# Optimization experiments

Measured on AMD Instinct MI355X. Metric: run time of the kernel, lower is better.

Reference implementation:

```python
import jax, jax.numpy as jnp
import numpy as np

B = 2048       # batch
N = 256        # num_memory_locations
M = 64         # memory_size
U = 512        # num_units
IN = 10        # num_bits_per_vector + 2
SHIFT = 1      # conv_shift_range
CLIP = 20.0


def setup_inputs() -> dict:
    key = jax.random.key(0)
    ks = jax.random.split(key, 20)
    s = 0.05
    A0 = jax.random.uniform(ks[5], (2, B, N), dtype=jnp.float32)
    A0 = A0 / jnp.sum(A0, axis=-1, keepdims=True)  # distribution-like prev attention
    return {
        'x_t':  jax.random.normal(ks[0], (B, IN), dtype=jnp.float32),
        'H0':   jax.random.normal(ks[1], (B, U), dtype=jnp.float32) * s,
        'C0':   jax.random.normal(ks[2], (B, U), dtype=jnp.float32) * s,
        'm0':   jax.random.normal(ks[3], (B, N, M), dtype=jnp.float32) * s,
        'R0':   jax.random.normal(ks[4], (B, M), dtype=jnp.float32) * s,
        'A0':   A0,
        'Wprep': jax.random.normal(ks[6], (M, U), dtype=jnp.float32) * s,
        'bprep': jnp.zeros((U,), dtype=jnp.float32),
        'Wx':   jax.random.normal(ks[7], (IN + U, 4 * U), dtype=jnp.float32) * s,
        'Wh':   jax.random.normal(ks[8], (U, 4 * U), dtype=jnp.float32) * s,
        'bl':   jnp.zeros((4 * U,), dtype=jnp.float32),
        'Wr':   jax.random.normal(ks[9], (U, M + 6), dtype=jnp.float32) * s,
        'br':   jnp.zeros((M + 6,), dtype=jnp.float32),
        'Ww':   jax.random.normal(ks[10], (U, 3 * M + 6), dtype=jnp.float32) * s,
        'bw':   jnp.zeros((3 * M + 6,), dtype=jnp.float32),
        'Wo':   jax.random.normal(ks[11], (U + M, U), dtype=jnp.float32) * s,
        'bo':   jnp.zeros((U,), dtype=jnp.float32),
    }


def _addressing(head, m_tm1, a_tm1):
    # head: (B, >=M+6); m_tm1: (B,N,M); a_tm1: (B,N)
    k = jnp.tanh(head[:, :M])                                   # (B,M)
    beta = jax.nn.softplus(head[:, M])                          # (B,)
    g = jax.nn.sigmoid(head[:, M + 1])                          # (B,)
    s = jax.nn.softmax(head[:, M + 2:M + 2 + 2 * SHIFT + 1], axis=-1)  # (B,3)
    gamma = jax.nn.softplus(head[:, M + 2 + 2 * SHIFT + 1])     # (B,)
    # cosine similarity content addressing
    ip = jnp.einsum('bnm,bm->bn', m_tm1, k)                     # (B,N)
    k_norm = jnp.sqrt(jnp.sum(k * k, axis=1, keepdims=True))    # (B,1)
    m_norm = jnp.sqrt(jnp.sum(m_tm1 * m_tm1, axis=2))           # (B,N)
    K = ip / (k_norm * m_norm + 1e-8)
    w_c = jax.nn.softmax(beta[:, None] * K, axis=1)             # exp/sum == softmax
    w_g = g[:, None] * w_c + (1.0 - g[:, None]) * a_tm1
    # circular convolution: s placed at offsets [0..SHIFT] and [-SHIFT..-1]
    s_full = jnp.concatenate(
        [s[:, :SHIFT + 1], jnp.zeros((s.shape[0], N - (2 * SHIFT + 1)), s.dtype), s[:, -SHIFT:]],
        axis=1)                                                 # (B,N)
    idx = (jnp.arange(N)[:, None] - jnp.arange(N)[None, :]) % N  # (N,N)
    w_conv = jnp.einsum('bij,bj->bi', s_full[:, idx], w_g)       # w[i]=sum_j w_g[j]*s[(i-j)%N]
    w_sharp = w_conv ** gamma[:, None]
    return w_sharp / jnp.sum(w_sharp, axis=1, keepdims=True)


def reference(x_t, H0, C0, m0, R0, A0, Wprep, bprep, Wx, Wh, bl, Wr, br, Ww, bw, Wo, bo):
    # prep from previous reads
    h = R0 @ Wprep + bprep                                      # (B,U)
    # single-layer LSTM controller
    z = jnp.concatenate([x_t, h], axis=1) @ Wx + H0 @ Wh + bl   # (B,4U)
    i, f, g_, o = jnp.split(z, 4, axis=1)
    c_t = jax.nn.sigmoid(f) * C0 + jax.nn.sigmoid(i) * jnp.tanh(g_)
    h = jax.nn.sigmoid(o) * jnp.tanh(c_t)
    h = jnp.clip(h, -CLIP, CLIP)
    # heads
    r_out = h @ Wr + br                                         # (B, M+6)
    w_out = h @ Ww + bw                                         # (B, 3M+6)
    w_read = _addressing(r_out, m0, A0[0])                      # (B,N)
    w_write = _addressing(w_out, m0, A0[1])                     # (B,N)
    # read from OLD memory (as in original)
    R_t = jnp.einsum('bn,bnm->bm', w_read, m0)                  # (B,M)
    # write: erase + add
    del_v = jax.nn.sigmoid(w_out[:, -2 * M:-M])                 # (B,M)
    add_v = jnp.tanh(w_out[:, -M:])                             # (B,M)
    ww = w_write[:, :, None]                                    # (B,N,1)
    m_t = m0 * (1.0 - ww * del_v[:, None, :]) + ww * add_v[:, None, :]
    y_t = jnp.clip(jnp.concatenate([h, R_t], axis=1) @ Wo + bo, -CLIP, CLIP)
    return (y_t, m_t, R_t, w_read, w_write)
```

## Files before the change

kernel.cpp:

```cpp
#include <hip/hip_runtime.h>


using u16   = unsigned short;
using bfrag = __attribute__((ext_vector_type(8))) short;
using f4    = __attribute__((ext_vector_type(4))) float;

__device__ __forceinline__ float bf2f(u16 s){ union{float f;unsigned u;}v; v.u=((unsigned)s)<<16; return v.f; }
__device__ __forceinline__ u16 f2bf(float f){ union{float f;unsigned u;}v; v.f=f; unsigned r=v.u+0x7fffu+((v.u>>16)&1u); return (u16)(r>>16); }
__device__ __forceinline__ void bfpair(unsigned pr, float&a, float&b){ union{float f;unsigned u;}x,y; x.u=pr<<16; y.u=pr&0xffff0000u; a=x.f; b=y.f; }
__device__ __forceinline__ unsigned packbf(float a, float b){ return (unsigned)f2bf(a) | ((unsigned)f2bf(b)<<16); }
__device__ __forceinline__ float sigm(float x){ return 1.f/(1.f+expf(-x)); }
__device__ __forceinline__ float softplus_(float x){ return fmaxf(x,0.f)+log1pf(expf(-fabsf(x))); }

__device__ __forceinline__ void gld16(const u16* g, u16* l){
    __builtin_amdgcn_global_load_lds((const __attribute__((address_space(1))) unsigned*)g,
                                     (__attribute__((address_space(3))) unsigned*)l, 16, 0, 0);
}


__global__ __launch_bounds__(256) void k_wt_lstm(const float* __restrict__ Wx, const float* __restrict__ Wh,
                                                 u16* __restrict__ Wt){
    __shared__ float t[32][33];
    int n0 = blockIdx.x*32, k0 = blockIdx.y*32;
    int tx = threadIdx.x & 31, ty = threadIdx.x >> 5;
    #pragma unroll
    for(int r=0;r<4;r++){
        int k = k0 + ty*4 + r, n = n0 + tx;
        float v;
        if(k < 522)       v = Wx[k*2048 + n];
        else if(k < 1034) v = Wh[(k-522)*2048 + n];
        else              v = 0.f;
        t[ty*4+r][tx] = v;
    }
    __syncthreads();
    #pragma unroll
    for(int r=0;r<4;r++){
        int n = n0 + ty*4 + r, k = k0 + tx;
        Wt[n*1056 + k] = f2bf(t[tx][ty*4+r]);
    }
}

__global__ __launch_bounds__(256) void k_wt_heads(const float* __restrict__ Wr, const float* __restrict__ Ww,
                                                  u16* __restrict__ Wt){
    __shared__ float t[32][33];
    int n0 = blockIdx.x*32, k0 = blockIdx.y*32;
    int tx = threadIdx.x & 31, ty = threadIdx.x >> 5;
    #pragma unroll
    for(int r=0;r<4;r++){
        int k = k0 + ty*4 + r, n = n0 + tx;
        float v;
        if(n < 70)        v = Wr[k*70 + n];
        else if(n < 268)  v = Ww[k*198 + (n-70)];
        else              v = 0.f;
        t[ty*4+r][tx] = v;
    }
    __syncthreads();
    #pragma unroll
    for(int r=0;r<4;r++){
        int n = n0 + ty*4 + r, k = k0 + tx;
        Wt[n*512 + k] = f2bf(t[tx][ty*4+r]);
    }
}

__global__ __launch_bounds__(256) void k_wt_out(const float* __restrict__ Wo, u16* __restrict__ Wt){
    __shared__ float t[32][33];
    int n0 = blockIdx.x*32, k0 = blockIdx.y*32;
    int tx = threadIdx.x & 31, ty = threadIdx.x >> 5;
    #pragma unroll
    for(int r=0;r<4;r++){
        int k = k0 + ty*4 + r, n = n0 + tx;
        t[ty*4+r][tx] = Wo[k*512 + n];
    }
    __syncthreads();
    #pragma unroll
    for(int r=0;r<4;r++){
        int n = n0 + ty*4 + r, k = k0 + tx;
        Wt[n*576 + k] = f2bf(t[tx][ty*4+r]);
    }
}

__global__ __launch_bounds__(256) void k_abuild(const float* __restrict__ x, const float* __restrict__ H0,
                                                const float* __restrict__ R0, const float* __restrict__ Wprep,
                                                const float* __restrict__ bprep, u16* __restrict__ A){
    int flat = blockIdx.x*256 + threadIdx.x;
    int b = flat >> 9, u = flat & 511;
    u16* Ab = A + (size_t)b*1056;
    float acc = bprep[u];
    const float* r = R0 + b*64;
    #pragma unroll 8
    for(int m=0;m<64;m++) acc += r[m] * Wprep[m*512+u];
    Ab[10+u] = f2bf(acc);
    Ab[522+u] = f2bf(H0[b*512+u]);
    if(u<10) Ab[u] = f2bf(x[b*10+u]);
    if(u<22) Ab[1034+u] = 0;
}

__device__ __forceinline__ void gemm128(const u16* __restrict__ A, int lda,
                                        const u16* __restrict__ Bt, int ldb,
                                        int bm, int bn, int kiters,
                                        u16* Al, u16* Bl, f4 acc[4][4]){
    int tid = threadIdx.x, w = tid>>6, lane = tid&63, quad = lane>>4, l16 = lane&15;
    int wr = w>>1, wc = w&1;
    f4 z4 = {0.f,0.f,0.f,0.f};
    #pragma unroll
    for(int i=0;i<4;i++)
        #pragma unroll
        for(int j=0;j<4;j++) acc[i][j] = z4;
    int rA0 = tid>>2, kc = tid&3;
    int rA1 = rA0 + 64;
    const u16* ga0 = A  + (size_t)(bm+rA0)*lda + kc*8;
    const u16* ga1 = A  + (size_t)(bm+rA1)*lda + kc*8;
    const u16* gb0 = Bt + (size_t)(bn+rA0)*ldb + kc*8;
    const u16* gb1 = Bt + (size_t)(bn+rA1)*ldb + kc*8;
    u16* lA0 = Al + (w*64)*8;
    u16* lA1 = Al + (256 + w*64)*8;
    u16* lB0 = Bl + (w*64)*8;
    u16* lB1 = Bl + (256 + w*64)*8;
    for(int kt=0; kt<kiters; kt++){
        __syncthreads();
        gld16(ga0, lA0); gld16(ga1, lA1);
        gld16(gb0, lB0); gld16(gb1, lB1);
        ga0 += 32; ga1 += 32; gb0 += 32; gb1 += 32;
        __syncthreads();
        bfrag af[4], bf[4];
        #pragma unroll
        for(int i=0;i<4;i++) af[i] = *(const bfrag*)&Al[(wr*64 + i*16 + l16)*32 + quad*8];
        #pragma unroll
        for(int j=0;j<4;j++) bf[j] = *(const bfrag*)&Bl[(wc*64 + j*16 + l16)*32 + quad*8];
        #pragma unroll
        for(int i=0;i<4;i++)
            #pragma unroll
            for(int j=0;j<4;j++)
                acc[i][j] = __builtin_amdgcn_mfma_f32_16x16x32_bf16(af[i], bf[j], acc[i][j], 0, 0, 0);
    }
}

__global__ __launch_bounds__(256) void k_gemm_lstm(const u16* __restrict__ A, const u16* __restrict__ Wt,
                                                   float* __restrict__ z){
    __shared__ u16 Al[128*32], Bl[128*32];
    f4 acc[4][4];
    int bm = blockIdx.x*128, bn = blockIdx.y*128;
    gemm128(A, 1056, Wt, 1056, bm, bn, 33, Al, Bl, acc);
    int lane = threadIdx.x&63, quad = lane>>4, l16 = lane&15, w = threadIdx.x>>6;
    int wr = w>>1, wc = w&1;
    #pragma unroll
    for(int i=0;i<4;i++){
        #pragma unroll
        for(int j=0;j<4;j++){
            int col = bn + wc*64 + j*16 + l16;
            #pragma unroll
            for(int r=0;r<4;r++){
                int row = bm + wr*64 + i*16 + quad*4 + r;
                z[(size_t)row*2048 + col] = acc[i][j][r];
            }
        }
    }
}

__global__ __launch_bounds__(256) void k_gates(const float* __restrict__ z, const float* __restrict__ C0,
                                               const float* __restrict__ bl, u16* __restrict__ A2){
    int flat = blockIdx.x*256 + threadIdx.x;
    int b = flat>>9, u = flat&511;
    const float* zb = z + (size_t)b*2048;
    float zi = zb[u]      + bl[u];
    float zf = zb[512+u]  + bl[512+u];
    float zg = zb[1024+u] + bl[1024+u];
    float zo = zb[1536+u] + bl[1536+u];
    float c  = sigm(zf)*C0[b*512+u] + sigm(zi)*tanhf(zg);
    float hv = sigm(zo)*tanhf(c);
    hv = fminf(fmaxf(hv,-20.f),20.f);
    A2[(size_t)b*576 + u] = f2bf(hv);
}

__global__ __launch_bounds__(256) void k_gemm_heads(const u16* __restrict__ A2, const u16* __restrict__ Wt,
                                                    const float* __restrict__ br, const float* __restrict__ bw,
                                                    float* __restrict__ rout, float* __restrict__ wout){
    __shared__ u16 Al[128*32], Bl[128*32];
    f4 acc[4][4];
    int bm = blockIdx.x*128, bn = blockIdx.y*128;
    gemm128(A2, 576, Wt, 512, bm, bn, 16, Al, Bl, acc);
    int lane = threadIdx.x&63, quad = lane>>4, l16 = lane&15, w = threadIdx.x>>6;
    int wr = w>>1, wc = w&1;
    #pragma unroll
    for(int i=0;i<4;i++){
        #pragma unroll
        for(int j=0;j<4;j++){
            int col = bn + wc*64 + j*16 + l16;
            if(col >= 268) continue;
            #pragma unroll
            for(int r=0;r<4;r++){
                int row = bm + wr*64 + i*16 + quad*4 + r;
                float v = acc[i][j][r];
                if(col < 70) rout[(size_t)row*70 + col]        = v + br[col];
                else         wout[(size_t)row*198 + (col-70)]  = v + bw[col-70];
            }
        }
    }
}

__global__ __launch_bounds__(256) void k_gemm_out(const u16* __restrict__ A2, const u16* __restrict__ Wt,
                                                  const float* __restrict__ bo, float* __restrict__ y){
    __shared__ u16 Al[128*32], Bl[128*32];
    f4 acc[4][4];
    int bm = blockIdx.x*128, bn = blockIdx.y*128;
    gemm128(A2, 576, Wt, 576, bm, bn, 18, Al, Bl, acc);
    int lane = threadIdx.x&63, quad = lane>>4, l16 = lane&15, w = threadIdx.x>>6;
    int wr = w>>1, wc = w&1;
    #pragma unroll
    for(int i=0;i<4;i++){
        #pragma unroll
        for(int j=0;j<4;j++){
            int col = bn + wc*64 + j*16 + l16;
            float bias = bo[col];
            #pragma unroll
            for(int r=0;r<4;r++){
                int row = bm + wr*64 + i*16 + quad*4 + r;
                float v = acc[i][j][r] + bias;
                v = fminf(fmaxf(v,-20.f),20.f);
                y[(size_t)row*512 + col] = v;
            }
        }
    }
}

__global__ __launch_bounds__(256, 4) void k_addr(const float* __restrict__ m0, const float* __restrict__ A0,
                                              const float* __restrict__ rout, const float* __restrict__ wout,
                                              u16* __restrict__ A2,
                                              float* __restrict__ out_mt, float* __restrict__ out_rt,
                                              float* __restrict__ out_wr, float* __restrict__ out_ww){
    __shared__ __align__(16) float kk_s[2][64];
    __shared__ float knorm_s[2];
    __shared__ float sc[2][6];
    __shared__ float ipbuf[3][256];
    __shared__ float wgrr[512];
    __shared__ float wsel[2][256];
    __shared__ __align__(16) float dv[64], avv[64];
    __shared__ float wpart[4][6];
    int tid = threadIdx.x, b = blockIdx.x;
    int lane = tid & 63, w = tid >> 6;
    int g = tid >> 4, c = tid & 15, mc = c*4;

    float a0r = A0[b*256 + tid];
    float a1r = A0[524288 + b*256 + tid];

    float4 v[16];
    const float* mb = m0 + (size_t)b*16384;
    #pragma unroll
    for(int i=0;i<16;i++) v[i] = *(const float4*)(mb + i*1024 + tid*4);

    if(tid < 128){
        int hh = tid >> 6, m = lane;
        float kv = tanhf(hh ? wout[b*198 + m] : rout[b*70 + m]);
        kk_s[hh][m] = kv;
        float s2 = kv*kv;
        #pragma unroll
        for(int o=32;o>0;o>>=1) s2 += __shfl_xor(s2, o, 64);
        if(m == 0) knorm_s[hh] = sqrtf(s2);
    } else if(tid < 192){
        int hh = tid - 128;
        if(hh < 2){
            const float* hd = hh ? (wout + b*198) : (rout + b*70);
            sc[hh][0] = softplus_(hd[64]);
            sc[hh][1] = sigm(hd[65]);
            float e0=hd[66], e1=hd[67], e2=hd[68];
            float mx = fmaxf(e0, fmaxf(e1, e2));
            float x0=expf(e0-mx), x1=expf(e1-mx), x2=expf(e2-mx);
            float ssum = x0+x1+x2;
            sc[hh][2]=x0/ssum; sc[hh][3]=x1/ssum; sc[hh][4]=x2/ssum;
            sc[hh][5] = softplus_(hd[69]);
        }
    } else {
        int m = tid - 192;
        dv[m]  = sigm(wout[b*198 + 70 + m]);
        avv[m] = tanhf(wout[b*198 + 134 + m]);
    }
    __syncthreads();

    {
        float4 ka = *(const float4*)&kk_s[0][mc];
        float4 kb = *(const float4*)&kk_s[1][mc];
        float rip0=0.f, rip1=0.f, rssq=0.f;
        #pragma unroll
        for(int i=0;i<16;i++){
            float4 t = v[i];
            float p0 = t.x*ka.x + t.y*ka.y + t.z*ka.z + t.w*ka.w;
            float p1 = t.x*kb.x + t.y*kb.y + t.z*kb.z + t.w*kb.w;
            float ps = t.x*t.x + t.y*t.y + t.z*t.z + t.w*t.w;
            #pragma unroll
            for(int o=1;o<16;o<<=1){
                p0 += __shfl_xor(p0, o);
                p1 += __shfl_xor(p1, o);
                ps += __shfl_xor(ps, o);
            }
            if(c == i){ rip0 = p0; rip1 = p1; rssq = ps; }
        }
        int idx = c*16 + g;
        ipbuf[0][idx] = rip0;
        ipbuf[1][idx] = rip1;
        ipbuf[2][idx] = rssq;
    }
    __syncthreads();
    float ip0 = ipbuf[0][tid], ip1 = ipbuf[1][tid], ssq = ipbuf[2][tid];

    float mn = sqrtf(ssq);
    float K0 = ip0 / (knorm_s[0]*mn + 1e-8f);
    float K1 = ip1 / (knorm_s[1]*mn + 1e-8f);
    float e0 = sc[0][0]*K0, e1 = sc[1][0]*K1;

    float mx0 = e0, mx1 = e1;
    #pragma unroll
    for(int o=32;o>0;o>>=1){ mx0 = fmaxf(mx0, __shfl_xor(mx0,o,64)); mx1 = fmaxf(mx1, __shfl_xor(mx1,o,64)); }
    if(lane == 0){ wpart[w][0] = mx0; wpart[w][1] = mx1; }
    __syncthreads();
    mx0 = fmaxf(fmaxf(wpart[0][0],wpart[1][0]), fmaxf(wpart[2][0],wpart[3][0]));
    mx1 = fmaxf(fmaxf(wpart[0][1],wpart[1][1]), fmaxf(wpart[2][1],wpart[3][1]));
    float p0 = expf(e0-mx0), p1 = expf(e1-mx1);
    float s0 = p0, s1 = p1;
    #pragma unroll
    for(int o=32;o>0;o>>=1){ s0 += __shfl_xor(s0,o,64); s1 += __shfl_xor(s1,o,64); }
    if(lane == 0){ wpart[w][2] = s0; wpart[w][3] = s1; }
    __syncthreads();
    s0 = wpart[0][2]+wpart[1][2]+wpart[2][2]+wpart[3][2];
    s1 = wpart[0][3]+wpart[1][3]+wpart[2][3]+wpart[3][3];
    float wc0 = p0/s0, wc1 = p1/s1;

    float g0 = sc[0][1], g1 = sc[1][1];
    float wg0 = g0*wc0 + (1.f-g0)*a0r;
    float wg1 = g1*wc1 + (1.f-g1)*a1r;
    wgrr[tid] = wg0; wgrr[256+tid] = wg1;
    __syncthreads();
    int nm1 = (tid+255)&255, np1 = (tid+1)&255;
    float conv0 = sc[0][2]*wg0 + sc[0][3]*wgrr[nm1]     + sc[0][4]*wgrr[np1];
    float conv1 = sc[1][2]*wg1 + sc[1][3]*wgrr[256+nm1] + sc[1][4]*wgrr[256+np1];
    conv0 = fmaxf(conv0, 1e-35f);  conv1 = fmaxf(conv1, 1e-35f);
    float wsh0 = expf(sc[0][5]*logf(conv0));
    float wsh1 = expf(sc[1][5]*logf(conv1));
    float t0 = wsh0, t1 = wsh1;
    #pragma unroll
    for(int o=32;o>0;o>>=1){ t0 += __shfl_xor(t0,o,64); t1 += __shfl_xor(t1,o,64); }
    if(lane == 0){ wpart[w][4] = t0; wpart[w][5] = t1; }
    __syncthreads();
    t0 = wpart[0][4]+wpart[1][4]+wpart[2][4]+wpart[3][4];
    t1 = wpart[0][5]+wpart[1][5]+wpart[2][5]+wpart[3][5];
    float w0 = wsh0/t0, w1 = wsh1/t1;
    wsel[0][tid] = w0; wsel[1][tid] = w1;
    out_wr[b*256 + tid] = w0;
    out_ww[b*256 + tid] = w1;
    __syncthreads();

    float r0=0.f, r1=0.f, r2=0.f, r3=0.f;
    {
        float d0=dv[mc], d1=dv[mc+1], d2=dv[mc+2], d3=dv[mc+3];
        float A0v=avv[mc], A1v=avv[mc+1], A2v=avv[mc+2], A3v=avv[mc+3];
        float* outb = out_mt + (size_t)b*16384;
        #pragma unroll
        for(int i=0;i<16;i++){
            int n = i*16 + g;
            float wwv = wsel[1][n], wrv = wsel[0][n];
            float4 t = v[i];
            float4 o;
            o.x = t.x*(1.f - wwv*d0) + wwv*A0v;
            o.y = t.y*(1.f - wwv*d1) + wwv*A1v;
            o.z = t.z*(1.f - wwv*d2) + wwv*A2v;
            o.w = t.w*(1.f - wwv*d3) + wwv*A3v;
            *(float4*)(outb + i*1024 + tid*4) = o;
            r0 += wrv*t.x; r1 += wrv*t.y; r2 += wrv*t.z; r3 += wrv*t.w;
        }
    }
    {
        float* rred = wgrr;
        if(g >= 8){
            rred[(g-8)*64 + mc]   = r0;
            rred[(g-8)*64 + mc+1] = r1;
            rred[(g-8)*64 + mc+2] = r2;
            rred[(g-8)*64 + mc+3] = r3;
        }
        __syncthreads();
        if(g < 8){
            rred[g*64 + mc]   += r0;
            rred[g*64 + mc+1] += r1;
            rred[g*64 + mc+2] += r2;
            rred[g*64 + mc+3] += r3;
        }
        __syncthreads();
        if(tid < 64){
            float rt = 0.f;
            #pragma unroll
            for(int g2=0; g2<8; g2++) rt += rred[g2*64 + tid];
            out_rt[b*64 + tid] = rt;
            A2[(size_t)b*576 + 512 + tid] = f2bf(rt);
        }
    }
}

extern "C" void kernel_launch(void* const* d_in, const int* in_sizes, int n_in,
                              void* d_out, int out_size, void* d_ws, size_t ws_size,
                              hipStream_t stream) {
    const float* x     = (const float*)d_in[0];
    const float* H0    = (const float*)d_in[1];
    const float* C0    = (const float*)d_in[2];
    const float* m0    = (const float*)d_in[3];
    const float* R0    = (const float*)d_in[4];
    const float* A0    = (const float*)d_in[5];
    const float* Wprep = (const float*)d_in[6];
    const float* bprep = (const float*)d_in[7];
    const float* Wx    = (const float*)d_in[8];
    const float* Wh    = (const float*)d_in[9];
    const float* bl    = (const float*)d_in[10];
    const float* Wr    = (const float*)d_in[11];
    const float* br    = (const float*)d_in[12];
    const float* Ww    = (const float*)d_in[13];
    const float* bw    = (const float*)d_in[14];
    const float* Wo    = (const float*)d_in[15];
    const float* bo    = (const float*)d_in[16];

    float* ws = (float*)d_ws;
    u16*   Wt_lstm = (u16*)(ws + 0);
    u16*   Wt_h    = (u16*)(ws + 1081344);
    u16*   Wt_o    = (u16*)(ws + 1179648);
    u16*   Abuf    = (u16*)(ws + 1327104);
    u16*   A2      = (u16*)(ws + 2408448);
    float* z       =        ws + 2998272;
    float* rout    =        ws + 7192576;
    float* wout    =        ws + 7335936;

    float* out    = (float*)d_out;
    float* out_y  = out;
    float* out_mt = out + 1048576;
    float* out_rt = out + 34603008;
    float* out_wr = out + 34734080;
    float* out_ww = out + 35258368;

    hipLaunchKernelGGL(k_wt_lstm,  dim3(64,33), dim3(256), 0, stream, Wx, Wh, Wt_lstm);
    hipLaunchKernelGGL(k_wt_heads, dim3(12,16), dim3(256), 0, stream, Wr, Ww, Wt_h);
    hipLaunchKernelGGL(k_wt_out,   dim3(16,18), dim3(256), 0, stream, Wo, Wt_o);
    hipLaunchKernelGGL(k_abuild,   dim3(4096),  dim3(256), 0, stream, x, H0, R0, Wprep, bprep, Abuf);
    hipLaunchKernelGGL(k_gemm_lstm, dim3(16,16), dim3(256), 0, stream, Abuf, Wt_lstm, z);
    hipLaunchKernelGGL(k_gates,    dim3(4096),  dim3(256), 0, stream, z, C0, bl, A2);
    hipLaunchKernelGGL(k_gemm_heads, dim3(16,3), dim3(256), 0, stream, A2, Wt_h, br, bw, rout, wout);
    hipLaunchKernelGGL(k_addr,     dim3(2048),  dim3(256), 0, stream, m0, A0, rout, wout, A2,
                       out_mt, out_rt, out_wr, out_ww);
    hipLaunchKernelGGL(k_gemm_out, dim3(16,4),  dim3(256), 0, stream, A2, Wt_o, bo, out_y);
}
```

Measured before the change: 391.7 us.

## Fuse LSTM gate activations into GEMM epilogue and merge prep kernels

Permutes the columns of the transposed LSTM weight so that each 64-column warp tile holds the i, f, g, o gates of the same 16 units. The gate nonlinearities can then be computed directly in the GEMM epilogue, which removes the fp32 z buffer round trip and the separate gates kernel. The three weight-transpose kernels and the A-build kernel are also merged into a single launch. This cuts launch overhead and roughly 32MB of z traffic, at the cost of uncoalesced C0 reads and scattered bf16 stores in the epilogue.

```diff
diff --git a/kernel.cpp b/kernel.cpp
--- a/kernel.cpp
+++ b/kernel.cpp
@@ -7,8 +7,6 @@
 
 __device__ __forceinline__ float bf2f(u16 s){ union{float f;unsigned u;}v; v.u=((unsigned)s)<<16; return v.f; }
 __device__ __forceinline__ u16 f2bf(float f){ union{float f;unsigned u;}v; v.f=f; unsigned r=v.u+0x7fffu+((v.u>>16)&1u); return (u16)(r>>16); }
-__device__ __forceinline__ void bfpair(unsigned pr, float&a, float&b){ union{float f;unsigned u;}x,y; x.u=pr<<16; y.u=pr&0xffff0000u; a=x.f; b=y.f; }
-__device__ __forceinline__ unsigned packbf(float a, float b){ return (unsigned)f2bf(a) | ((unsigned)f2bf(b)<<16); }
 __device__ __forceinline__ float sigm(float x){ return 1.f/(1.f+expf(-x)); }
 __device__ __forceinline__ float softplus_(float x){ return fmaxf(x,0.f)+log1pf(expf(-fabsf(x))); }
 
@@ -17,82 +15,81 @@
                                      (__attribute__((address_space(3))) unsigned*)l, 16, 0, 0);
 }
 
-
-__global__ __launch_bounds__(256) void k_wt_lstm(const float* __restrict__ Wx, const float* __restrict__ Wh,
-                                                 u16* __restrict__ Wt){
+__global__ __launch_bounds__(256) void k_prep(const float* __restrict__ Wx, const float* __restrict__ Wh,
+                                              const float* __restrict__ Wr, const float* __restrict__ Ww,
+                                              const float* __restrict__ Wo,
+                                              const float* __restrict__ x, const float* __restrict__ H0,
+                                              const float* __restrict__ R0, const float* __restrict__ Wprep,
+                                              const float* __restrict__ bprep,
+                                              u16* __restrict__ Wt_lstm, u16* __restrict__ Wt_h,
+                                              u16* __restrict__ Wt_o, u16* __restrict__ Abuf){
     __shared__ float t[32][33];
-    int n0 = blockIdx.x*32, k0 = blockIdx.y*32;
+    int bx = blockIdx.x;
     int tx = threadIdx.x & 31, ty = threadIdx.x >> 5;
-    #pragma unroll
-    for(int r=0;r<4;r++){
-        int k = k0 + ty*4 + r, n = n0 + tx;
-        float v;
-        if(k < 522)       v = Wx[k*2048 + n];
-        else if(k < 1034) v = Wh[(k-522)*2048 + n];
-        else              v = 0.f;
-        t[ty*4+r][tx] = v;
-    }
-    __syncthreads();
-    #pragma unroll
-    for(int r=0;r<4;r++){
-        int n = n0 + ty*4 + r, k = k0 + tx;
-        Wt[n*1056 + k] = f2bf(t[tx][ty*4+r]);
-    }
-}
-
-__global__ __launch_bounds__(256) void k_wt_heads(const float* __restrict__ Wr, const float* __restrict__ Ww,
-                                                  u16* __restrict__ Wt){
-    __shared__ float t[32][33];
-    int n0 = blockIdx.x*32, k0 = blockIdx.y*32;
-    int tx = threadIdx.x & 31, ty = threadIdx.x >> 5;
-    #pragma unroll
-    for(int r=0;r<4;r++){
-        int k = k0 + ty*4 + r, n = n0 + tx;
-        float v;
-        if(n < 70)        v = Wr[k*70 + n];
-        else if(n < 268)  v = Ww[k*198 + (n-70)];
-        else              v = 0.f;
-        t[ty*4+r][tx] = v;
-    }
-    __syncthreads();
-    #pragma unroll
-    for(int r=0;r<4;r++){
-        int n = n0 + ty*4 + r, k = k0 + tx;
-        Wt[n*512 + k] = f2bf(t[tx][ty*4+r]);
-    }
-}
-
-__global__ __launch_bounds__(256) void k_wt_out(const float* __restrict__ Wo, u16* __restrict__ Wt){
-    __shared__ float t[32][33];
-    int n0 = blockIdx.x*32, k0 = blockIdx.y*32;
-    int tx = threadIdx.x & 31, ty = threadIdx.x >> 5;
-    #pragma unroll
-    for(int r=0;r<4;r++){
-        int k = k0 + ty*4 + r, n = n0 + tx;
-        t[ty*4+r][tx] = Wo[k*512 + n];
-    }
-    __syncthreads();
-    #pragma unroll
-    for(int r=0;r<4;r++){
-        int n = n0 + ty*4 + r, k = k0 + tx;
-        Wt[n*576 + k] = f2bf(t[tx][ty*4+r]);
-    }
-}
-
-__global__ __launch_bounds__(256) void k_abuild(const float* __restrict__ x, const float* __restrict__ H0,
-                                                const float* __restrict__ R0, const float* __restrict__ Wprep,
-                                                const float* __restrict__ bprep, u16* __restrict__ A){
-    int flat = blockIdx.x*256 + threadIdx.x;
-    int b = flat >> 9, u = flat & 511;
-    u16* Ab = A + (size_t)b*1056;
-    float acc = bprep[u];
-    const float* r = R0 + b*64;
-    #pragma unroll 8
-    for(int m=0;m<64;m++) acc += r[m] * Wprep[m*512+u];
-    Ab[10+u] = f2bf(acc);
-    Ab[522+u] = f2bf(H0[b*512+u]);
-    if(u<10) Ab[u] = f2bf(x[b*10+u]);
-    if(u<22) Ab[1034+u] = 0;
+    if(bx < 2112){
+        int n0 = (bx & 63)*32, k0 = (bx >> 6)*32;
+        #pragma unroll
+        for(int r=0;r<4;r++){
+            int k = k0 + ty*4 + r, n = n0 + tx;
+            float v;
+            if(k < 522)       v = Wx[k*2048 + n];
+            else if(k < 1034) v = Wh[(k-522)*2048 + n];
+            else              v = 0.f;
+            t[ty*4+r][tx] = v;
+        }
+        __syncthreads();
+        #pragma unroll
+        for(int r=0;r<4;r++){
+            int n = n0 + ty*4 + r, k = k0 + tx;
+            int u = n & 511, gate = n >> 9;
+            int np = ((u>>4)<<6) + (gate<<4) + (u&15);
+            Wt_lstm[np*1056 + k] = f2bf(t[tx][ty*4+r]);
+        }
+    } else if(bx < 2304){
+        int idx = bx - 2112;
+        int n0 = (idx % 12)*32, k0 = (idx / 12)*32;
+        #pragma unroll
+        for(int r=0;r<4;r++){
+            int k = k0 + ty*4 + r, n = n0 + tx;
+            float v;
+            if(n < 70)        v = Wr[k*70 + n];
+            else if(n < 268)  v = Ww[k*198 + (n-70)];
+            else              v = 0.f;
+            t[ty*4+r][tx] = v;
+        }
+        __syncthreads();
+        #pragma unroll
+        for(int r=0;r<4;r++){
+            int n = n0 + ty*4 + r, k = k0 + tx;
+            Wt_h[n*512 + k] = f2bf(t[tx][ty*4+r]);
+        }
+    } else if(bx < 2592){
+        int idx = bx - 2304;
+        int n0 = (idx % 16)*32, k0 = (idx / 16)*32;
+        #pragma unroll
+        for(int r=0;r<4;r++){
+            int k = k0 + ty*4 + r, n = n0 + tx;
+            t[ty*4+r][tx] = Wo[k*512 + n];
+        }
+        __syncthreads();
+        #pragma unroll
+        for(int r=0;r<4;r++){
+            int n = n0 + ty*4 + r, k = k0 + tx;
+            Wt_o[n*576 + k] = f2bf(t[tx][ty*4+r]);
+        }
+    } else {
+        int flat = (bx - 2592)*256 + threadIdx.x;
+        int b = flat >> 9, u = flat & 511;
+        u16* Ab = Abuf + (size_t)b*1056;
+        float acc = bprep[u];
+        const float* r = R0 + b*64;
+        #pragma unroll 8
+        for(int m=0;m<64;m++) acc += r[m] * Wprep[m*512+u];
+        Ab[10+u] = f2bf(acc);
+        Ab[522+u] = f2bf(H0[b*512+u]);
+        if(u<10) Ab[u] = f2bf(x[b*10+u]);
+        if(u<22) Ab[1034+u] = 0;
+    }
 }
 
 __device__ __forceinline__ void gemm128(const u16* __restrict__ A, int lda,
@@ -136,40 +133,31 @@
 }
 
 __global__ __launch_bounds__(256) void k_gemm_lstm(const u16* __restrict__ A, const u16* __restrict__ Wt,
-                                                   float* __restrict__ z){
+                                                   const float* __restrict__ C0, const float* __restrict__ bl,
+                                                   u16* __restrict__ A2){
     __shared__ u16 Al[128*32], Bl[128*32];
     f4 acc[4][4];
     int bm = blockIdx.x*128, bn = blockIdx.y*128;
     gemm128(A, 1056, Wt, 1056, bm, bn, 33, Al, Bl, acc);
     int lane = threadIdx.x&63, quad = lane>>4, l16 = lane&15, w = threadIdx.x>>6;
     int wr = w>>1, wc = w&1;
+    int u = (((bn + wc*64)>>6)<<4) + l16;
+    float bi = bl[u], bff = bl[512+u], bg = bl[1024+u], bo_ = bl[1536+u];
     #pragma unroll
     for(int i=0;i<4;i++){
         #pragma unroll
-        for(int j=0;j<4;j++){
-            int col = bn + wc*64 + j*16 + l16;
-            #pragma unroll
-            for(int r=0;r<4;r++){
-                int row = bm + wr*64 + i*16 + quad*4 + r;
-                z[(size_t)row*2048 + col] = acc[i][j][r];
-            }
-        }
-    }
-}
-
-__global__ __launch_bounds__(256) void k_gates(const float* __restrict__ z, const float* __restrict__ C0,
-                                               const float* __restrict__ bl, u16* __restrict__ A2){
-    int flat = blockIdx.x*256 + threadIdx.x;
-    int b = flat>>9, u = flat&511;
-    const float* zb = z + (size_t)b*2048;
-    float zi = zb[u]      + bl[u];
-    float zf = zb[512+u]  + bl[512+u];
-    float zg = zb[1024+u] + bl[1024+u];
-    float zo = zb[1536+u] + bl[1536+u];
-    float c  = sigm(zf)*C0[b*512+u] + sigm(zi)*tanhf(zg);
-    float hv = sigm(zo)*tanhf(c);
-    hv = fminf(fmaxf(hv,-20.f),20.f);
-    A2[(size_t)b*576 + u] = f2bf(hv);
+        for(int r=0;r<4;r++){
+            int b = bm + wr*64 + i*16 + quad*4 + r;
+            float zi = acc[i][0][r] + bi;
+            float zf = acc[i][1][r] + bff;
+            float zg = acc[i][2][r] + bg;
+            float zo = acc[i][3][r] + bo_;
+            float c  = sigm(zf)*C0[b*512+u] + sigm(zi)*tanhf(zg);
+            float hv = sigm(zo)*tanhf(c);
+            hv = fminf(fmaxf(hv,-20.f),20.f);
+            A2[(size_t)b*576 + u] = f2bf(hv);
+        }
+    }
 }
 
 __global__ __launch_bounds__(256) void k_gemm_heads(const u16* __restrict__ A2, const u16* __restrict__ Wt,
@@ -420,9 +408,8 @@
     u16*   Wt_o    = (u16*)(ws + 1179648);
     u16*   Abuf    = (u16*)(ws + 1327104);
     u16*   A2      = (u16*)(ws + 2408448);
-    float* z       =        ws + 2998272;
-    float* rout    =        ws + 7192576;
-    float* wout    =        ws + 7335936;
+    float* rout    =        ws + 2998272;
+    float* wout    =        ws + 3141632;
 
     float* out    = (float*)d_out;
     float* out_y  = out;
@@ -431,14 +418,12 @@
     float* out_wr = out + 34734080;
     float* out_ww = out + 35258368;
 
-    hipLaunchKernelGGL(k_wt_lstm,  dim3(64,33), dim3(256), 0, stream, Wx, Wh, Wt_lstm);
-    hipLaunchKernelGGL(k_wt_heads, dim3(12,16), dim3(256), 0, stream, Wr, Ww, Wt_h);
-    hipLaunchKernelGGL(k_wt_out,   dim3(16,18), dim3(256), 0, stream, Wo, Wt_o);
-    hipLaunchKernelGGL(k_abuild,   dim3(4096),  dim3(256), 0, stream, x, H0, R0, Wprep, bprep, Abuf);
-    hipLaunchKernelGGL(k_gemm_lstm, dim3(16,16), dim3(256), 0, stream, Abuf, Wt_lstm, z);
-    hipLaunchKernelGGL(k_gates,    dim3(4096),  dim3(256), 0, stream, z, C0, bl, A2);
+    hipLaunchKernelGGL(k_prep,      dim3(6688), dim3(256), 0, stream,
+                       Wx, Wh, Wr, Ww, Wo, x, H0, R0, Wprep, bprep,
+                       Wt_lstm, Wt_h, Wt_o, Abuf);
+    hipLaunchKernelGGL(k_gemm_lstm, dim3(16,16), dim3(256), 0, stream, Abuf, Wt_lstm, C0, bl, A2);
     hipLaunchKernelGGL(k_gemm_heads, dim3(16,3), dim3(256), 0, stream, A2, Wt_h, br, bw, rout, wout);
-    hipLaunchKernelGGL(k_addr,     dim3(2048),  dim3(256), 0, stream, m0, A0, rout, wout, A2,
+    hipLaunchKernelGGL(k_addr,      dim3(2048),  dim3(256), 0, stream, m0, A0, rout, wout, A2,
                        out_mt, out_rt, out_wr, out_ww);
-    hipLaunchKernelGGL(k_gemm_out, dim3(16,4),  dim3(256), 0, stream, A2, Wt_o, bo, out_y);
-}
+    hipLaunchKernelGGL(k_gemm_out,  dim3(16,4),  dim3(256), 0, stream, A2, Wt_o, bo, out_y);
+}
```

After: 379.9 us. 1.03x faster.
